# Performance work log

Measured on AMD Instinct MI355X. Metric: run time of the kernel, lower is better.

The kernel has to match this reference:

```python
import jax, jax.numpy as jnp
import numpy as np


def _linear_interp_last(x, out_size):
    """1D linear interpolation along last axis, matching F.interpolate
    (align_corners=False): src = (dst + 0.5) * scale - 0.5, clamped."""
    C = x.shape[-1]
    scale = C / out_size
    pos = jnp.clip((jnp.arange(out_size, dtype=x.dtype) + 0.5) * scale - 0.5, 0.0, C - 1)
    lo = jnp.floor(pos).astype(jnp.int32)
    hi = jnp.minimum(lo + 1, C - 1)
    w = pos - lo.astype(x.dtype)
    return jnp.take(x, lo, axis=-1) * (1.0 - w) + jnp.take(x, hi, axis=-1) * w


def setup_inputs() -> dict:
    key = jax.random.key(0)
    k1, k2, k3, k4, k5 = jax.random.split(key, 5)
    B, C, H, W, K, S = 16, 128, 128, 128, 256, 1024
    return {
        "shape": jax.random.normal(k1, (B, C, H, W), jnp.float32),
        "size": S,
        "saliency": jax.random.uniform(k2, (B, 1, H, W), jnp.float32),
        "mask": jax.random.randint(k3, (B, K), 0, 2, jnp.int32),
        "ind": jax.random.randint(k4, (B, K), 0, H * W, jnp.int32),
        "target": jax.random.normal(k5, (B, K, S), jnp.float32),
    }


def reference(shape, size, saliency, mask, ind, target):
    B, C, H, W = shape.shape
    K = ind.shape[1]
    # [B,C,H,W] -> [B,HW,C]
    feat = shape.transpose(0, 2, 3, 1).reshape(B, H * W, C)
    # gather per-object features: [B,K,C]
    idx = jnp.broadcast_to(ind[:, :, None], (B, K, C))
    pred = jnp.take_along_axis(feat, idx, axis=1)
    # resize channel dim C -> size (linear interp; torch code's 'bilinear' on 3D)
    pred = _linear_interp_last(pred, size)  # [B,K,size]
    m = mask.astype(pred.dtype)[:, :, None]  # [B,K,1], broadcast over size
    loss = jnp.sum(jnp.abs(pred * m - target * m))
    denom = jnp.sum(m) * size + 1e-4  # sum of mask expanded to [B,K,size]
    return loss / denom
```

## Files before the change

kernel.cpp:

```cpp
#include <hip/hip_runtime.h>

#define B_ 16
#define C_ 128
#define H_ 128
#define W_ 128
#define K_ 256
#define S_ 1024
#define BK_   (B_ * K_)
#define PAIRS 4
#define NBLK  (BK_ / PAIRS)

__global__ __launch_bounds__(256) void maskloss_main(
    const float* __restrict__ shape,
    const int*   __restrict__ mask,
    const int*   __restrict__ ind,
    const float* __restrict__ target,
    float*       __restrict__ partial,
    int*         __restrict__ counts)
{
    const int blk = blockIdx.x;
    const int bk0 = blk * PAIRS;
    const int b   = bk0 >> 8;
    const int tid = threadIdx.x;

    __shared__ int   sMask[PAIRS];
    __shared__ int   sInd[PAIRS];
    __shared__ float pred[PAIRS][C_];

    if (tid < PAIRS) {
        sMask[tid] = mask[bk0 + tid];
        sInd[tid]  = ind[bk0 + tid];
    }
    __syncthreads();

    const int nact = sMask[0] + sMask[1] + sMask[2] + sMask[3];
    if (nact == 0) {
        if (tid == 0) { partial[blk] = 0.f; counts[blk] = 0; }
        return;
    }

    const size_t planeB = (size_t)b * (C_ * H_ * W_);
#pragma unroll
    for (int j = 0; j < (PAIRS * C_) / 256; ++j) {
        const int slot = tid + j * 256;
        const int p    = slot >> 7;
        const int c    = slot & (C_ - 1);
        if (sMask[p])
            pred[p][c] = shape[planeB + (size_t)c * (H_ * W_) + sInd[p]];
    }
    __syncthreads();

    float acc = 0.f;
#pragma unroll
    for (int p = 0; p < PAIRS; ++p) {
        if (!sMask[p]) continue;
        const float4 t =
            reinterpret_cast<const float4*>(target + (size_t)(bk0 + p) * S_)[tid];
        const float* pr = pred[p];
        float v[4];
#pragma unroll
        for (int j = 0; j < 4; ++j) {
            const int s = 4 * tid + j;
            float pp = fmaf((float)s, 0.125f, -0.4375f);
            pp = fminf(fmaxf(pp, 0.f), 127.f);
            const int   lo = (int)pp;
            const float w  = pp - (float)lo;
            const int   hi = min(lo + 1, C_ - 1);
            v[j] = pr[lo] * (1.f - w) + pr[hi] * w;
        }
        acc += fabsf(v[0] - t.x) + fabsf(v[1] - t.y)
             + fabsf(v[2] - t.z) + fabsf(v[3] - t.w);
    }

    for (int off = 32; off > 0; off >>= 1)
        acc += __shfl_down(acc, off, 64);
    __shared__ float wsum[4];
    if ((tid & 63) == 0) wsum[tid >> 6] = acc;
    __syncthreads();
    if (tid == 0) {
        partial[blk] = (wsum[0] + wsum[1]) + (wsum[2] + wsum[3]);
        counts[blk]  = nact;
    }
}

__global__ __launch_bounds__(1024) void maskloss_final(
    const float* __restrict__ partial,
    const int*   __restrict__ counts,
    float*       __restrict__ out)
{
    const int tid = threadIdx.x;
    double lsum = (double)partial[tid];
    int    csum = counts[tid];
    for (int off = 32; off > 0; off >>= 1) {
        lsum += __shfl_down(lsum, off, 64);
        csum += __shfl_down(csum, off, 64);
    }
    __shared__ double lw[16];
    __shared__ int    cw[16];
    if ((tid & 63) == 0) { lw[tid >> 6] = lsum; cw[tid >> 6] = csum; }
    __syncthreads();
    if (tid == 0) {
        double L = 0.0; int Cn = 0;
#pragma unroll
        for (int i = 0; i < 16; ++i) { L += lw[i]; Cn += cw[i]; }
        out[0] = (float)(L / ((double)Cn * (double)S_ + 1e-4));
    }
}

extern "C" void kernel_launch(void* const* d_in, const int* in_sizes, int n_in,
                              void* d_out, int out_size, void* d_ws, size_t ws_size,
                              hipStream_t stream) {
    const float* shape  = (const float*)d_in[0];
    const int*   mask   = (const int*)d_in[3];
    const int*   ind    = (const int*)d_in[4];
    const float* target = (const float*)d_in[5];
    float*       out    = (float*)d_out;

    float* partial = (float*)d_ws;
    int*   counts  = (int*)d_ws + NBLK;

    maskloss_main<<<NBLK, 256, 0, stream>>>(shape, mask, ind, target, partial, counts);
    maskloss_final<<<1, 1024, 0, stream>>>(partial, counts, out);
}
```

Baseline: 190.5 us.

## Fuse final reduction via last-block ticket and prefetch target before gather

The separate final reduction kernel is replaced by an atomic ticket counter, so the last block to finish reduces all partials inside the main kernel. Target loads are also issued before the scattered shape gather, so both memory streams are in flight together. This removes a kernel launch but adds a memset launch plus a device-wide threadfence and atomic per block.

```diff
diff --git a/kernel.cpp b/kernel.cpp
--- a/kernel.cpp
+++ b/kernel.cpp
@@ -10,13 +10,15 @@
 #define PAIRS 4
 #define NBLK  (BK_ / PAIRS)
 
-__global__ __launch_bounds__(256) void maskloss_main(
+__global__ __launch_bounds__(256) void maskloss_fused(
     const float* __restrict__ shape,
     const int*   __restrict__ mask,
     const int*   __restrict__ ind,
     const float* __restrict__ target,
     float*       __restrict__ partial,
-    int*         __restrict__ counts)
+    int*         __restrict__ counts,
+    unsigned int* __restrict__ ticket,
+    float*       __restrict__ out)
 {
     const int blk = blockIdx.x;
     const int bk0 = blk * PAIRS;
@@ -34,42 +36,47 @@
     __syncthreads();
 
     const int nact = sMask[0] + sMask[1] + sMask[2] + sMask[3];
-    if (nact == 0) {
-        if (tid == 0) { partial[blk] = 0.f; counts[blk] = 0; }
-        return;
-    }
-
-    const size_t planeB = (size_t)b * (C_ * H_ * W_);
-#pragma unroll
-    for (int j = 0; j < (PAIRS * C_) / 256; ++j) {
-        const int slot = tid + j * 256;
-        const int p    = slot >> 7;
-        const int c    = slot & (C_ - 1);
-        if (sMask[p])
-            pred[p][c] = shape[planeB + (size_t)c * (H_ * W_) + sInd[p]];
-    }
-    __syncthreads();
 
     float acc = 0.f;
+    if (nact) {
+        float4 t[PAIRS];
 #pragma unroll
-    for (int p = 0; p < PAIRS; ++p) {
-        if (!sMask[p]) continue;
-        const float4 t =
-            reinterpret_cast<const float4*>(target + (size_t)(bk0 + p) * S_)[tid];
-        const float* pr = pred[p];
-        float v[4];
+        for (int p = 0; p < PAIRS; ++p)
+            if (sMask[p])
+                t[p] = reinterpret_cast<const float4*>(
+                           target + (size_t)(bk0 + p) * S_)[tid];
+
+        const size_t planeB = (size_t)b * (C_ * H_ * W_);
 #pragma unroll
-        for (int j = 0; j < 4; ++j) {
-            const int s = 4 * tid + j;
-            float pp = fmaf((float)s, 0.125f, -0.4375f);
-            pp = fminf(fmaxf(pp, 0.f), 127.f);
-            const int   lo = (int)pp;
-            const float w  = pp - (float)lo;
-            const int   hi = min(lo + 1, C_ - 1);
-            v[j] = pr[lo] * (1.f - w) + pr[hi] * w;
+        for (int j = 0; j < (PAIRS * C_) / 256; ++j) {
+            const int slot = tid + j * 256;
+            const int p    = slot >> 7;
+            const int c    = slot & (C_ - 1);
+            if (sMask[p])
+                pred[p][c] = shape[planeB + (size_t)c * (H_ * W_) + sInd[p]];
         }
-        acc += fabsf(v[0] - t.x) + fabsf(v[1] - t.y)
-             + fabsf(v[2] - t.z) + fabsf(v[3] - t.w);
+        __syncthreads();
+
+#pragma unroll
+        for (int p = 0; p < PAIRS; ++p) {
+            if (!sMask[p]) continue;
+            const float* pr = pred[p];
+            float v[4];
+#pragma unroll
+            for (int j = 0; j < 4; ++j) {
+                const int s = 4 * tid + j;
+                float pp = fmaf((float)s, 0.125f, -0.4375f);
+                pp = fminf(fmaxf(pp, 0.f), 127.f);
+                const int   lo = (int)pp;
+                const float w  = pp - (float)lo;
+                const int   hi = min(lo + 1, C_ - 1);
+                v[j] = pr[lo] * (1.f - w) + pr[hi] * w;
+            }
+            acc += fabsf(v[0] - t[p].x) + fabsf(v[1] - t[p].y)
+                 + fabsf(v[2] - t[p].z) + fabsf(v[3] - t[p].w);
+        }
+    } else {
+        __syncthreads();
     }
 
     for (int off = 32; off > 0; off >>= 1)
@@ -77,32 +84,38 @@
     __shared__ float wsum[4];
     if ((tid & 63) == 0) wsum[tid >> 6] = acc;
     __syncthreads();
+
+    __shared__ bool isLast;
     if (tid == 0) {
         partial[blk] = (wsum[0] + wsum[1]) + (wsum[2] + wsum[3]);
         counts[blk]  = nact;
+        __threadfence();
+        isLast = (atomicAdd(ticket, 1u) == NBLK - 1);
     }
-}
+    __syncthreads();
+    if (!isLast) return;
 
-__global__ __launch_bounds__(1024) void maskloss_final(
-    const float* __restrict__ partial,
-    const int*   __restrict__ counts,
-    float*       __restrict__ out)
-{
-    const int tid = threadIdx.x;
-    double lsum = (double)partial[tid];
-    int    csum = counts[tid];
+    __threadfence();
+    const volatile float* vp = partial;
+    const volatile int*   vc = counts;
+    double lsum = 0.0; int csum = 0;
+#pragma unroll
+    for (int i = 0; i < NBLK / 256; ++i) {
+        const int j = tid + i * 256;
+        lsum += (double)vp[j];
+        csum += vc[j];
+    }
     for (int off = 32; off > 0; off >>= 1) {
         lsum += __shfl_down(lsum, off, 64);
         csum += __shfl_down(csum, off, 64);
     }
-    __shared__ double lw[16];
-    __shared__ int    cw[16];
+    __shared__ double lw[4];
+    __shared__ int    cw[4];
     if ((tid & 63) == 0) { lw[tid >> 6] = lsum; cw[tid >> 6] = csum; }
     __syncthreads();
     if (tid == 0) {
-        double L = 0.0; int Cn = 0;
-#pragma unroll
-        for (int i = 0; i < 16; ++i) { L += lw[i]; Cn += cw[i]; }
+        const double L  = (lw[0] + lw[1]) + (lw[2] + lw[3]);
+        const int    Cn = (cw[0] + cw[1]) + (cw[2] + cw[3]);
         out[0] = (float)(L / ((double)Cn * (double)S_ + 1e-4));
     }
 }
@@ -116,9 +129,11 @@
     const float* target = (const float*)d_in[5];
     float*       out    = (float*)d_out;
 
-    float* partial = (float*)d_ws;
-    int*   counts  = (int*)d_ws + NBLK;
+    float*        partial = (float*)d_ws;
+    int*          counts  = (int*)((char*)d_ws + NBLK * 4);
+    unsigned int* ticket  = (unsigned int*)((char*)d_ws + 2 * NBLK * 4);
 
-    maskloss_main<<<NBLK, 256, 0, stream>>>(shape, mask, ind, target, partial, counts);
-    maskloss_final<<<1, 1024, 0, stream>>>(partial, counts, out);
+    hipMemsetAsync(ticket, 0, sizeof(unsigned int), stream);
+    maskloss_fused<<<NBLK, 256, 0, stream>>>(shape, mask, ind, target,
+                                             partial, counts, ticket, out);
 }
```

Measured after the change: 231.9 us. 1.22x slower.
